# Performance work log

Hardware: AMD Instinct MI355X
Metric: run time of the kernel (lower is better)

Reference implementation:

```python
import jax, jax.numpy as jnp
import numpy as np

N = 4_000_000      # total rows across all strata
D = 64             # covariate dimension (nn.Linear input_size)
N_SEG = 100_000    # number of strata (groups)


def setup_inputs() -> dict:
    key = jax.random.key(0)
    k1, k2, k3, k4 = jax.random.split(key, 4)
    X = jax.random.normal(k1, (N, D), dtype=jnp.float32)
    # sorted segment ids encode the ragged strata lengths (rows are packed per group)
    seg_ids = jnp.sort(jax.random.randint(k2, (N,), 0, N_SEG)).astype(jnp.int32)
    w = jax.random.normal(k3, (D,), dtype=jnp.float32) * 0.1
    b = jax.random.normal(k4, (1,), dtype=jnp.float32)
    return {"X": X, "seg_ids": seg_ids, "w": w, "b": b}


def reference(X, seg_ids, w, b):
    # linear projection to a single logit per row: y_hat = X @ w + b
    logits = X @ w + b[0]                                   # [N]
    # segment softmax == padded (-300) row softmax with padding underflowing to 0
    m = jax.ops.segment_max(logits, seg_ids, num_segments=N_SEG)   # [N_SEG]
    m = jnp.where(jnp.isfinite(m), m, jnp.float32(0.0))            # guard empty segments
    z = jnp.exp(logits - m[seg_ids])                               # [N]
    denom = jax.ops.segment_sum(z, seg_ids, num_segments=N_SEG)    # [N_SEG]
    return z / denom[seg_ids]                                      # [N] per-group softmax probs
```

## Files before the change

kernel.cpp:

```cpp
#include <hip/hip_runtime.h>
#include <math.h>

#define NROWS 4000000
#define DCOV  64
#define NSEG  100000

#define LOGITS_BLOCKS 2048
#define BOUNDS_BLOCKS 512

typedef float f32x4 __attribute__((ext_vector_type(4)));

__global__ void fused_logits_bounds_kernel(const float* __restrict__ X,
                                           const float* __restrict__ w,
                                           const float* __restrict__ b,
                                           const int* __restrict__ seg,
                                           float* __restrict__ logits,
                                           int* __restrict__ st) {
    if (blockIdx.x < LOGITS_BLOCKS) {
        const int lane        = threadIdx.x & 63;
        const int waveInBlock = threadIdx.x >> 6;
        const int sub         = lane & 15;
        const int rowInGroup  = lane >> 4;

        const long long nwaves = (long long)LOGITS_BLOCKS * 4;
        const long long gwave  = (long long)blockIdx.x * 4 + waveInBlock;
        const long long npairs = NROWS / 8;

        const float4 w4 = reinterpret_cast<const float4*>(w)[sub];
        const float bias = b[0];

        const f32x4* Xv = reinterpret_cast<const f32x4*>(X);

        for (long long p = gwave; p < npairs; p += nwaves) {
            const f32x4* xp = Xv + p * 128;
            f32x4 x0 = __builtin_nontemporal_load(xp + lane);
            f32x4 x1 = __builtin_nontemporal_load(xp + 64 + lane);
            float p0 = x0.x * w4.x + x0.y * w4.y + x0.z * w4.z + x0.w * w4.w;
            float p1 = x1.x * w4.x + x1.y * w4.y + x1.z * w4.z + x1.w * w4.w;
            p0 += __shfl_xor(p0, 1);  p1 += __shfl_xor(p1, 1);
            p0 += __shfl_xor(p0, 2);  p1 += __shfl_xor(p1, 2);
            p0 += __shfl_xor(p0, 4);  p1 += __shfl_xor(p1, 4);
            p0 += __shfl_xor(p0, 8);  p1 += __shfl_xor(p1, 8);
            if (sub == 0) {
                logits[p * 8 + rowInGroup]     = p0 + bias;
                logits[p * 8 + 4 + rowInGroup] = p1 + bias;
            }
        }
    } else {
        const long long tid    = (long long)(blockIdx.x - LOGITS_BLOCKS) * blockDim.x
                               + threadIdx.x;
        const long long stride = (long long)BOUNDS_BLOCKS * blockDim.x;
        for (long long i = tid; i < NROWS; i += stride) {
            int s = seg[i];
            if (i == 0) {
                for (int t = 0; t <= s; ++t) st[t] = 0;
            } else {
                int prev = seg[i - 1];
                for (int t = prev + 1; t <= s; ++t) st[t] = (int)i;
            }
            if (i == NROWS - 1) {
                for (int t = s + 1; t <= NSEG; ++t) st[t] = NROWS;
            }
        }
    }
}

__global__ void seg_softmax_kernel(const float* __restrict__ logits,
                                   const int* __restrict__ st,
                                   float* __restrict__ out, int nseg) {
    const int lane = threadIdx.x & 63;
    const int wave = threadIdx.x >> 6;
    const int s = blockIdx.x * (blockDim.x >> 6) + wave;
    if (s >= nseg) return;

    const int start = st[s];
    const int end   = st[s + 1];
    const int len   = end - start;

    if (len <= 64) {
        const bool act = lane < len;
        float x = act ? logits[start + lane] : -INFINITY;
        float mx = x;
        #pragma unroll
        for (int m = 1; m < 64; m <<= 1) mx = fmaxf(mx, __shfl_xor(mx, m));
        float e = act ? __expf(x - mx) : 0.0f;
        float sum = e;
        #pragma unroll
        for (int m = 1; m < 64; m <<= 1) sum += __shfl_xor(sum, m);
        if (act) out[start + lane] = e / sum;
    } else {
        float mx = -INFINITY;
        for (int i = start + lane; i < end; i += 64) mx = fmaxf(mx, logits[i]);
        #pragma unroll
        for (int m = 1; m < 64; m <<= 1) mx = fmaxf(mx, __shfl_xor(mx, m));
        float sum = 0.0f;
        for (int i = start + lane; i < end; i += 64) sum += __expf(logits[i] - mx);
        #pragma unroll
        for (int m = 1; m < 64; m <<= 1) sum += __shfl_xor(sum, m);
        const float inv = 1.0f / sum;
        for (int i = start + lane; i < end; i += 64)
            out[i] = __expf(logits[i] - mx) * inv;
    }
}

extern "C" void kernel_launch(void* const* d_in, const int* in_sizes, int n_in,
                              void* d_out, int out_size, void* d_ws, size_t ws_size,
                              hipStream_t stream) {
    const float* X   = (const float*)d_in[0];
    const int*   seg = (const int*)d_in[1];
    const float* w   = (const float*)d_in[2];
    const float* b   = (const float*)d_in[3];
    float*       out = (float*)d_out;

    float* logits = (float*)d_ws;
    int*   st     = (int*)((char*)d_ws + (size_t)NROWS * sizeof(float));

    fused_logits_bounds_kernel<<<LOGITS_BLOCKS + BOUNDS_BLOCKS, 256, 0, stream>>>(
        X, w, b, seg, logits, st);

    const int wavesPerBlock = 4;
    const int nblocks = (NSEG + wavesPerBlock - 1) / wavesPerBlock;
    seg_softmax_kernel<<<nblocks, wavesPerBlock * 64, 0, stream>>>(
        logits, st, out, NSEG);
}
```

Baseline: 216.9 us.

## Fuse logits, segment bounds and segment softmax into one per-segment-block kernel

Each block takes 25 consecutive segments and finds its row range by binary search over the sorted segment ids. It then computes segment starts in LDS, computes logits into an LDS buffer, and runs the per-segment softmax from LDS before writing the output. This drops the global logits round trip and the second kernel launch. The cost is a serial binary search per block, uneven load across blocks, and a global fallback path when a block's rows exceed the LDS capacity.

```diff
diff --git a/kernel.cpp b/kernel.cpp
--- a/kernel.cpp
+++ b/kernel.cpp
@@ -5,101 +5,141 @@
 #define DCOV  64
 #define NSEG  100000
 
-#define LOGITS_BLOCKS 2048
-#define BOUNDS_BLOCKS 512
+#define SEGS_PER_BLOCK 25
+#define NBLOCKS (NSEG / SEGS_PER_BLOCK)
+#define CAP 2048
 
 typedef float f32x4 __attribute__((ext_vector_type(4)));
 
-__global__ void fused_logits_bounds_kernel(const float* __restrict__ X,
-                                           const float* __restrict__ w,
-                                           const float* __restrict__ b,
-                                           const int* __restrict__ seg,
-                                           float* __restrict__ logits,
-                                           int* __restrict__ st) {
-    if (blockIdx.x < LOGITS_BLOCKS) {
-        const int lane        = threadIdx.x & 63;
-        const int waveInBlock = threadIdx.x >> 6;
-        const int sub         = lane & 15;
-        const int rowInGroup  = lane >> 4;
+__global__ __launch_bounds__(256, 8)
+void fused_clr_kernel(const float* __restrict__ X,
+                      const int* __restrict__ seg,
+                      const float* __restrict__ w,
+                      const float* __restrict__ b,
+                      float* __restrict__ out,
+                      float* __restrict__ gl ) {
+    __shared__ int   st_lds[SEGS_PER_BLOCK + 1];
+    __shared__ float logit_lds[CAP];
+    __shared__ int   rs_sh, re_sh;
 
-        const long long nwaves = (long long)LOGITS_BLOCKS * 4;
-        const long long gwave  = (long long)blockIdx.x * 4 + waveInBlock;
-        const long long npairs = NROWS / 8;
+    const int tid  = threadIdx.x;
+    const int lane = tid & 63;
+    const int wv   = tid >> 6;
+    const int sub  = lane & 15;
+    const int rig  = lane >> 4;
 
-        const float4 w4 = reinterpret_cast<const float4*>(w)[sub];
-        const float bias = b[0];
+    const int s0 = blockIdx.x * SEGS_PER_BLOCK;
+    const int s1 = s0 + SEGS_PER_BLOCK;
 
-        const f32x4* Xv = reinterpret_cast<const f32x4*>(X);
+    if (tid < 2) {
+        const int target = (tid == 0) ? s0 : s1;
+        int lo = 0, hi = NROWS;
+        while (lo < hi) {
+            int mid = (lo + hi) >> 1;
+            if (seg[mid] < target) lo = mid + 1; else hi = mid;
+        }
+        if (tid == 0) rs_sh = lo; else re_sh = lo;
+    }
+    __syncthreads();
+    const int row_start = rs_sh;
+    const int row_end   = re_sh;
+    const int nrows     = row_end - row_start;
 
-        for (long long p = gwave; p < npairs; p += nwaves) {
-            const f32x4* xp = Xv + p * 128;
-            f32x4 x0 = __builtin_nontemporal_load(xp + lane);
-            f32x4 x1 = __builtin_nontemporal_load(xp + 64 + lane);
-            float p0 = x0.x * w4.x + x0.y * w4.y + x0.z * w4.z + x0.w * w4.w;
-            float p1 = x1.x * w4.x + x1.y * w4.y + x1.z * w4.z + x1.w * w4.w;
-            p0 += __shfl_xor(p0, 1);  p1 += __shfl_xor(p1, 1);
-            p0 += __shfl_xor(p0, 2);  p1 += __shfl_xor(p1, 2);
-            p0 += __shfl_xor(p0, 4);  p1 += __shfl_xor(p1, 4);
-            p0 += __shfl_xor(p0, 8);  p1 += __shfl_xor(p1, 8);
-            if (sub == 0) {
-                logits[p * 8 + rowInGroup]     = p0 + bias;
-                logits[p * 8 + 4 + rowInGroup] = p1 + bias;
-            }
+    for (int j = tid; j <= SEGS_PER_BLOCK; j += 256) st_lds[j] = row_end;
+    __syncthreads();
+    for (int i = row_start + tid; i < row_end; i += 256) {
+        int s    = seg[i];
+        int prev = (i == row_start) ? (s0 - 1) : seg[i - 1];
+        for (int t = prev + 1; t <= s; ++t) st_lds[t - s0] = i;
+    }
+
+    const bool  use_lds = (nrows <= CAP);
+    const float bias    = b[0];
+    const float4 w4     = reinterpret_cast<const float4*>(w)[sub];
+    const f32x4* Xv     = reinterpret_cast<const f32x4*>(X);
+
+    __syncthreads();
+
+    for (int rb = row_start + wv * 16; rb < row_end; rb += 64) {
+        const int r0 = rb + rig, r1 = rb + 4 + rig, r2 = rb + 8 + rig, r3 = rb + 12 + rig;
+        f32x4 x0 = {0,0,0,0}, x1 = {0,0,0,0}, x2 = {0,0,0,0}, x3 = {0,0,0,0};
+        const f32x4* xp = Xv + (long long)rb * 16 + lane;
+        if (r0 < row_end) x0 = __builtin_nontemporal_load(xp);
+        if (r1 < row_end) x1 = __builtin_nontemporal_load(xp + 64);
+        if (r2 < row_end) x2 = __builtin_nontemporal_load(xp + 128);
+        if (r3 < row_end) x3 = __builtin_nontemporal_load(xp + 192);
+        float p0 = x0.x * w4.x + x0.y * w4.y + x0.z * w4.z + x0.w * w4.w;
+        float p1 = x1.x * w4.x + x1.y * w4.y + x1.z * w4.z + x1.w * w4.w;
+        float p2 = x2.x * w4.x + x2.y * w4.y + x2.z * w4.z + x2.w * w4.w;
+        float p3 = x3.x * w4.x + x3.y * w4.y + x3.z * w4.z + x3.w * w4.w;
+        #pragma unroll
+        for (int m = 1; m < 16; m <<= 1) {
+            p0 += __shfl_xor(p0, m);
+            p1 += __shfl_xor(p1, m);
+            p2 += __shfl_xor(p2, m);
+            p3 += __shfl_xor(p3, m);
         }
-    } else {
-        const long long tid    = (long long)(blockIdx.x - LOGITS_BLOCKS) * blockDim.x
-                               + threadIdx.x;
-        const long long stride = (long long)BOUNDS_BLOCKS * blockDim.x;
-        for (long long i = tid; i < NROWS; i += stride) {
-            int s = seg[i];
-            if (i == 0) {
-                for (int t = 0; t <= s; ++t) st[t] = 0;
+        if (sub == 0) {
+            if (use_lds) {
+                if (r0 < row_end) logit_lds[r0 - row_start] = p0 + bias;
+                if (r1 < row_end) logit_lds[r1 - row_start] = p1 + bias;
+                if (r2 < row_end) logit_lds[r2 - row_start] = p2 + bias;
+                if (r3 < row_end) logit_lds[r3 - row_start] = p3 + bias;
             } else {
-                int prev = seg[i - 1];
-                for (int t = prev + 1; t <= s; ++t) st[t] = (int)i;
-            }
-            if (i == NROWS - 1) {
-                for (int t = s + 1; t <= NSEG; ++t) st[t] = NROWS;
+                if (r0 < row_end) gl[r0] = p0 + bias;
+                if (r1 < row_end) gl[r1] = p1 + bias;
+                if (r2 < row_end) gl[r2] = p2 + bias;
+                if (r3 < row_end) gl[r3] = p3 + bias;
             }
         }
     }
-}
+    __syncthreads();
 
-__global__ void seg_softmax_kernel(const float* __restrict__ logits,
-                                   const int* __restrict__ st,
-                                   float* __restrict__ out, int nseg) {
-    const int lane = threadIdx.x & 63;
-    const int wave = threadIdx.x >> 6;
-    const int s = blockIdx.x * (blockDim.x >> 6) + wave;
-    if (s >= nseg) return;
+    for (int j = wv; j < SEGS_PER_BLOCK; j += 4) {
+        const int a0  = st_lds[j];
+        const int a1  = st_lds[j + 1];
+        const int len = a1 - a0;
+        if (len <= 0) continue;
+        if (len <= 64) {
+            const bool act = lane < len;
+            const int  idx = a0 - row_start + lane;
+            float x = act ? (use_lds ? logit_lds[idx] : gl[a0 + lane]) : -INFINITY;
+            float mx = x;
+            #pragma unroll
+            for (int m = 1; m < 64; m <<= 1) mx = fmaxf(mx, __shfl_xor(mx, m));
+            float e = act ? __expf(x - mx) : 0.0f;
+            float sum = e;
+            #pragma unroll
+            for (int m = 1; m < 64; m <<= 1) sum += __shfl_xor(sum, m);
+            const float pr = e / sum;
+            if (act) {
+                if (use_lds) logit_lds[idx] = pr;
+                else         out[a0 + lane] = pr;
+            }
+        } else {
+            float mx = -INFINITY;
+            for (int i = a0 + lane; i < a1; i += 64)
+                mx = fmaxf(mx, use_lds ? logit_lds[i - row_start] : gl[i]);
+            #pragma unroll
+            for (int m = 1; m < 64; m <<= 1) mx = fmaxf(mx, __shfl_xor(mx, m));
+            float sum = 0.0f;
+            for (int i = a0 + lane; i < a1; i += 64)
+                sum += __expf((use_lds ? logit_lds[i - row_start] : gl[i]) - mx);
+            #pragma unroll
+            for (int m = 1; m < 64; m <<= 1) sum += __shfl_xor(sum, m);
+            const float inv = 1.0f / sum;
+            for (int i = a0 + lane; i < a1; i += 64) {
+                float pr = __expf((use_lds ? logit_lds[i - row_start] : gl[i]) - mx) * inv;
+                if (use_lds) logit_lds[i - row_start] = pr;
+                else         out[i] = pr;
+            }
+        }
+    }
+    __syncthreads();
 
-    const int start = st[s];
-    const int end   = st[s + 1];
-    const int len   = end - start;
-
-    if (len <= 64) {
-        const bool act = lane < len;
-        float x = act ? logits[start + lane] : -INFINITY;
-        float mx = x;
-        #pragma unroll
-        for (int m = 1; m < 64; m <<= 1) mx = fmaxf(mx, __shfl_xor(mx, m));
-        float e = act ? __expf(x - mx) : 0.0f;
-        float sum = e;
-        #pragma unroll
-        for (int m = 1; m < 64; m <<= 1) sum += __shfl_xor(sum, m);
-        if (act) out[start + lane] = e / sum;
-    } else {
-        float mx = -INFINITY;
-        for (int i = start + lane; i < end; i += 64) mx = fmaxf(mx, logits[i]);
-        #pragma unroll
-        for (int m = 1; m < 64; m <<= 1) mx = fmaxf(mx, __shfl_xor(mx, m));
-        float sum = 0.0f;
-        for (int i = start + lane; i < end; i += 64) sum += __expf(logits[i] - mx);
-        #pragma unroll
-        for (int m = 1; m < 64; m <<= 1) sum += __shfl_xor(sum, m);
-        const float inv = 1.0f / sum;
-        for (int i = start + lane; i < end; i += 64)
-            out[i] = __expf(logits[i] - mx) * inv;
+    if (use_lds) {
+        for (int i = tid; i < nrows; i += 256)
+            out[row_start + i] = logit_lds[i];
     }
 }
 
@@ -111,15 +151,7 @@
     const float* w   = (const float*)d_in[2];
     const float* b   = (const float*)d_in[3];
     float*       out = (float*)d_out;
+    float*       gl  = (float*)d_ws;
 
-    float* logits = (float*)d_ws;
-    int*   st     = (int*)((char*)d_ws + (size_t)NROWS * sizeof(float));
-
-    fused_logits_bounds_kernel<<<LOGITS_BLOCKS + BOUNDS_BLOCKS, 256, 0, stream>>>(
-        X, w, b, seg, logits, st);
-
-    const int wavesPerBlock = 4;
-    const int nblocks = (NSEG + wavesPerBlock - 1) / wavesPerBlock;
-    seg_softmax_kernel<<<nblocks, wavesPerBlock * 64, 0, stream>>>(
-        logits, st, out, NSEG);
+    fused_clr_kernel<<<NBLOCKS, 256, 0, stream>>>(X, seg, w, b, out, gl);
 }
```

Measured after the change: 185.4 us. 14.5% less time.
